# Optimization experiments

Hardware: AMD Instinct MI355X
Metric: run time of the kernel (lower is better)

## Reference

```python
import jax, jax.numpy as jnp
import numpy as np

C = 128          # hidden_channels
H = 8            # num_heads
D = C // H       # head dim = 16
OUT = 64         # out_channels
L = 2            # num_layers
NN = (30000, 60000, 6000)                 # poi, road, region node counts
NE = (200000, 300000, 200000, 100000)     # edges per edge type
ETS = ((0, 1), (1, 1), (1, 2), (2, 0))    # (src_type, dst_type) per edge type


def setup_inputs():
    key = jax.random.key(0)
    ks = iter(jax.random.split(key, 40))
    s = 1.0 / np.sqrt(C)
    sd = 1.0 / np.sqrt(D)
    inp = {}
    inp['x_poi'] = jax.random.normal(next(ks), (NN[0], C), jnp.float32)
    inp['x_road'] = jax.random.normal(next(ks), (NN[1], C), jnp.float32)
    inp['x_region'] = jax.random.normal(next(ks), (NN[2], C), jnp.float32)
    for et, (si, di) in enumerate(ETS):
        inp[f'e{et}_src'] = jax.random.randint(next(ks), (NE[et],), 0, NN[si], jnp.int32)
        inp[f'e{et}_dst'] = jax.random.randint(next(ks), (NE[et],), 0, NN[di], jnp.int32)
    # per-node-type input projection
    inp['lin_w'] = jax.random.normal(next(ks), (3, C, C), jnp.float32) * s
    inp['lin_b'] = jax.random.normal(next(ks), (3, C), jnp.float32) * 0.01
    # per-layer, per-node-type K/Q/V and output projections
    for nm in ('kw', 'qw', 'vw', 'aw'):
        inp[nm] = jax.random.normal(next(ks), (L, 3, C, C), jnp.float32) * s
    for nm in ('kb', 'qb', 'vb', 'ab'):
        inp[nm] = jax.random.normal(next(ks), (L, 3, C), jnp.float32) * 0.01
    # per-layer, per-edge-type relation matrices and priors
    inp['a_rel'] = jax.random.normal(next(ks), (L, 4, H, D, D), jnp.float32) * sd
    inp['m_rel'] = jax.random.normal(next(ks), (L, 4, H, D, D), jnp.float32) * sd
    inp['p_rel'] = jnp.ones((L, 4, H), jnp.float32)
    inp['skip'] = jnp.ones((L, 3), jnp.float32)
    inp['out_w'] = jax.random.normal(next(ks), (C, OUT), jnp.float32) * s
    inp['out_b'] = jnp.zeros((OUT,), jnp.float32)
    return inp


def _seg_softmax(alpha, dst, n):
    amax = jax.lax.stop_gradient(jax.ops.segment_max(alpha, dst, num_segments=n))
    ex = jnp.exp(alpha - amax[dst])
    den = jax.ops.segment_sum(ex, dst, num_segments=n)
    return ex / (den[dst] + 1e-16)


def _hgt_forward(xs, edges, lin_w, lin_b, kw, kb, qw, qb, vw, vb, aw, ab,
                 a_rel, m_rel, p_rel, skip, out_w, out_b):
    # per-node-type input linear + relu
    xs = [jax.nn.relu(xs[i] @ lin_w[i] + lin_b[i]) for i in range(3)]
    scale = 1.0 / np.sqrt(D)
    for l in range(L):
        k = [(xs[i] @ kw[l, i] + kb[l, i]).reshape(-1, H, D) for i in range(3)]
        q = [(xs[i] @ qw[l, i] + qb[l, i]).reshape(-1, H, D) for i in range(3)]
        v = [(xs[i] @ vw[l, i] + vb[l, i]).reshape(-1, H, D) for i in range(3)]
        agg = [jnp.zeros((NN[i], H, D), xs[i].dtype) for i in range(3)]
        for et, (si, di) in enumerate(ETS):
            src, dst = edges[et]
            n = NN[di]
            ke = jnp.einsum('ehd,hdf->ehf', k[si][src], a_rel[l, et])   # [E,H,D]
            alpha = jnp.einsum('ehd,ehd->eh', q[di][dst], ke) * p_rel[l, et] * scale
            alpha = _seg_softmax(alpha, dst, n)                          # [E,H]
            m = jnp.einsum('ehd,hdf->ehf', v[si][src], m_rel[l, et])    # [E,H,D]
            agg[di] = agg[di] + jax.ops.segment_sum(m * alpha[..., None], dst, num_segments=n)
        new_xs = []
        for i in range(3):
            o = jax.nn.gelu(agg[i].reshape(-1, C)) @ aw[l, i] + ab[l, i]
            beta = jax.nn.sigmoid(skip[l, i])
            o = beta * o + (1.0 - beta) * xs[i]
            new_xs.append(jax.nn.relu(o))  # HGT applies activation after each conv
        xs = new_xs
    return (xs[0] @ out_w + out_b, xs[1] @ out_w + out_b, xs[2] @ out_w + out_b)


def reference(x_poi, x_road, x_region,
              e0_src, e0_dst, e1_src, e1_dst, e2_src, e2_dst, e3_src, e3_dst,
              lin_w, lin_b, kw, kb, qw, qb, vw, vb, aw, ab,
              a_rel, m_rel, p_rel, skip, out_w, out_b):
    edges = ((e0_src, e0_dst), (e1_src, e1_dst), (e2_src, e2_dst), (e3_src, e3_dst))
    return _hgt_forward([x_poi, x_road, x_region], edges,
                        lin_w, lin_b, kw, kb, qw, qb, vw, vb, aw, ab,
                        a_rel, m_rel, p_rel, skip, out_w, out_b)
```

## Files before the change

kernel.cpp:

```cpp
#include <hip/hip_runtime.h>
#include <cstddef>
#include <cstdint>


typedef __attribute__((ext_vector_type(8))) short short8;
typedef __attribute__((ext_vector_type(4))) float floatx4;

__device__ __forceinline__ float gelu_fast(float x) {
    float u = 1.5957691216057308f * x * (1.0f + 0.044715f * x * x);
    return x / (1.0f + __expf(-u));
}

__device__ __forceinline__ unsigned short f2bf(float f) {
    unsigned u = __float_as_uint(f);
    u += 0x7fffu + ((u >> 16) & 1);
    return (unsigned short)(u >> 16);
}

__device__ __forceinline__ float bf2f(unsigned short h) {
    return __uint_as_float((unsigned)h << 16);
}

__device__ __forceinline__ void up8(uint4 u, float* f) {
    f[0] = __uint_as_float(u.x << 16); f[1] = __uint_as_float(u.x & 0xffff0000u);
    f[2] = __uint_as_float(u.y << 16); f[3] = __uint_as_float(u.y & 0xffff0000u);
    f[4] = __uint_as_float(u.z << 16); f[5] = __uint_as_float(u.z & 0xffff0000u);
    f[6] = __uint_as_float(u.w << 16); f[7] = __uint_as_float(u.w & 0xffff0000u);
}

__device__ __forceinline__ uint4 pk8(const float* f) {
    uint4 u;
    u.x = (unsigned)f2bf(f[0]) | ((unsigned)f2bf(f[1]) << 16);
    u.y = (unsigned)f2bf(f[2]) | ((unsigned)f2bf(f[3]) << 16);
    u.z = (unsigned)f2bf(f[4]) | ((unsigned)f2bf(f[5]) << 16);
    u.w = (unsigned)f2bf(f[6]) | ((unsigned)f2bf(f[7]) << 16);
    return u;
}

__global__ __launch_bounds__(256) void gemm_proj_all(
    const unsigned short* __restrict__ xs_bf,
    const unsigned short* __restrict__ Wl,
    const float* __restrict__ bl,
    unsigned short* __restrict__ proj)
{
    const int    NN_[3]  = {30000, 60000, 6000};
    const int    OFFr[3] = {0, 30000, 90000};
    const int    WOFF[3] = {0, 49152, 131072};
    const int    BOFF[3] = {0, 384, 1024};
    const size_t POFF[3] = {0, 11520000u, 49920000u};
    const int    LDO[3]  = {384, 640, 384};

    int by = blockIdx.x, t, lb;
    if (by < 2345)      { t = 1; lb = by; }
    else if (by < 3050) { t = 0; lb = by - 2345; }
    else                { t = 2; lb = by - 3050; }
    int XG = (t == 1) ? 5 : 3;
    int byy = lb / XG, bx = lb - byy * XG;

    const unsigned short* Abf = xs_bf + (size_t)OFFr[t] * 128;
    const unsigned short* Wt  = Wl + WOFF[t];
    const float* bias = bl + BOFF[t];
    unsigned short* outbf = proj + POFF[t];
    const int ldo = LDO[t], Nrows = NN_[t];

    const int wave = threadIdx.x >> 6, lane = threadIdx.x & 63;
    const int quad = lane >> 4, l16 = lane & 15;
    const int rowStart = (byy * 4 + wave) * 32;
    if (rowStart >= Nrows) return;
    short8 Afr[2][4];
    #pragma unroll
    for (int rt = 0; rt < 2; ++rt) {
        int m = rowStart + rt * 16 + l16;
        const unsigned short* ap = Abf + (size_t)((m < Nrows) ? m : 0) * 128 + quad * 8;
        #pragma unroll
        for (int kc = 0; kc < 4; ++kc)
            Afr[rt][kc] = *(const short8*)(ap + kc * 32);
    }
    int ct0 = bx * 2, ct1 = ct0 + 2;
    for (int ct = ct0; ct < ct1; ++ct) {
        int colBase = ct * 64;
        const unsigned short* wp = Wt + (size_t)(colBase + l16) * 128 + quad * 8;
        short8 B[4][4];
        #pragma unroll
        for (int c = 0; c < 4; ++c)
            #pragma unroll
            for (int kc = 0; kc < 4; ++kc)
                B[c][kc] = *(const short8*)(wp + (size_t)c * 2048 + kc * 32);
        floatx4 acc[2][4] = {{{0,0,0,0},{0,0,0,0},{0,0,0,0},{0,0,0,0}},
                             {{0,0,0,0},{0,0,0,0},{0,0,0,0},{0,0,0,0}}};
        #pragma unroll
        for (int kc = 0; kc < 4; ++kc)
            #pragma unroll
            for (int c = 0; c < 4; ++c) {
                acc[0][c] = __builtin_amdgcn_mfma_f32_16x16x32_bf16(B[c][kc], Afr[0][kc], acc[0][c], 0, 0, 0);
                acc[1][c] = __builtin_amdgcn_mfma_f32_16x16x32_bf16(B[c][kc], Afr[1][kc], acc[1][c], 0, 0, 0);
            }
        #pragma unroll
        for (int rt = 0; rt < 2; ++rt) {
            int node = rowStart + rt * 16 + l16;
            if (node >= Nrows) continue;
            #pragma unroll
            for (int c = 0; c < 4; ++c) {
                int col0 = colBase + c * 16 + quad * 4;
                float4 bv = *(const float4*)(bias + col0);
                uint2 u;
                u.x = (unsigned)f2bf(acc[rt][c][0] + bv.x) |
                      ((unsigned)f2bf(acc[rt][c][1] + bv.y) << 16);
                u.y = (unsigned)f2bf(acc[rt][c][2] + bv.z) |
                      ((unsigned)f2bf(acc[rt][c][3] + bv.w) << 16);
                *(uint2*)(outbf + (size_t)node * ldo + col0) = u;
            }
        }
    }
}

template<bool AF32, bool GIN, bool SKIP>
__global__ __launch_bounds__(256) void gemm_node(
    const void* __restrict__ a0v, const void* __restrict__ a1v, const void* __restrict__ a2v,
    const unsigned short* __restrict__ WtB, const float* __restrict__ biasB,
    const unsigned short* __restrict__ xoldB, const float* __restrict__ skipB,
    unsigned short* __restrict__ outB)
{
    const int TN[3]   = {30000, 60000, 6000};
    const int TOFF[3] = {0, 30000, 90000};
    int by = blockIdx.x;
    int t  = (by < 469) ? 0 : (by < 1407) ? 1 : 2;
    int lb = by - ((t == 0) ? 0 : (t == 1) ? 469 : 1407);
    int Nrows = TN[t];
    const void* av = (t == 0) ? a0v : (t == 1) ? a1v : a2v;
    const unsigned short* Wt = WtB + (size_t)t * 16384;
    const float* bias = biasB + t * 128;
    const unsigned short* xold = xoldB + (size_t)TOFF[t] * 128;
    unsigned short* out = outB + (size_t)TOFF[t] * 128;
    const int wave = threadIdx.x >> 6, lane = threadIdx.x & 63;
    const int quad = lane >> 4, l16 = lane & 15;
    const int rowStart = (lb * 4 + wave) * 16;
    if (rowStart >= Nrows) return;
    int m = rowStart + l16;
    size_t base = (size_t)((m < Nrows) ? m : 0) * 128 + quad * 8;
    short8 Afr[4];
    #pragma unroll
    for (int kc = 0; kc < 4; ++kc) {
        if (AF32) {
            const float* ap = (const float*)av + base;
            float4 f0 = *(const float4*)(ap + kc * 32);
            float4 f1 = *(const float4*)(ap + kc * 32 + 4);
            float af[8] = {f0.x, f0.y, f0.z, f0.w, f1.x, f1.y, f1.z, f1.w};
            short8 a;
            #pragma unroll
            for (int i = 0; i < 8; ++i) a[i] = (short)f2bf(af[i]);
            Afr[kc] = a;
        } else if (GIN) {
            const unsigned short* ap = (const unsigned short*)av + base;
            short8 a8 = *(const short8*)(ap + kc * 32);
            short8 a;
            #pragma unroll
            for (int i = 0; i < 8; ++i)
                a[i] = (short)f2bf(gelu_fast(bf2f((unsigned short)a8[i])));
            Afr[kc] = a;
        } else {
            const unsigned short* ap = (const unsigned short*)av + base;
            Afr[kc] = *(const short8*)(ap + kc * 32);
        }
    }
    float beta = 0.f, omb = 0.f;
    if (SKIP) { beta = 1.0f / (1.0f + __expf(-skipB[t])); omb = 1.0f - beta; }
    int node = rowStart + l16;
    bool ok = node < Nrows;
    #pragma unroll
    for (int ct = 0; ct < 2; ++ct) {
        int colBase = ct * 64;
        const unsigned short* wp = Wt + (size_t)(colBase + l16) * 128 + quad * 8;
        #pragma unroll
        for (int c = 0; c < 4; ++c) {
            floatx4 acc = {0, 0, 0, 0};
            #pragma unroll
            for (int kc = 0; kc < 4; ++kc) {
                short8 B = *(const short8*)(wp + (size_t)c * 2048 + kc * 32);
                acc = __builtin_amdgcn_mfma_f32_16x16x32_bf16(B, Afr[kc], acc, 0, 0, 0);
            }
            if (ok) {
                int col0 = colBase + c * 16 + quad * 4;
                float4 bv = *(const float4*)(bias + col0);
                float o0 = acc[0] + bv.x, o1 = acc[1] + bv.y;
                float o2 = acc[2] + bv.z, o3 = acc[3] + bv.w;
                if (SKIP) {
                    uint2 xo = *(const uint2*)(xold + (size_t)node * 128 + col0);
                    o0 = beta * o0 + omb * __uint_as_float(xo.x << 16);
                    o1 = beta * o1 + omb * __uint_as_float(xo.x & 0xffff0000u);
                    o2 = beta * o2 + omb * __uint_as_float(xo.y << 16);
                    o3 = beta * o3 + omb * __uint_as_float(xo.y & 0xffff0000u);
                }
                o0 = fmaxf(o0, 0.f); o1 = fmaxf(o1, 0.f);
                o2 = fmaxf(o2, 0.f); o3 = fmaxf(o3, 0.f);
                uint2 u;
                u.x = (unsigned)f2bf(o0) | ((unsigned)f2bf(o1) << 16);
                u.y = (unsigned)f2bf(o2) | ((unsigned)f2bf(o3) << 16);
                *(uint2*)(out + (size_t)node * 128 + col0) = u;
            }
        }
    }
}

__global__ __launch_bounds__(256) void gemm_out(
    const unsigned short* __restrict__ Abf,
    const unsigned short* __restrict__ Wt,
    const float* __restrict__ bias,
    float* __restrict__ out, int Nrows)
{
    const int wave = threadIdx.x >> 6, lane = threadIdx.x & 63;
    const int quad = lane >> 4, l16 = lane & 15;
    const int rowBase = (blockIdx.x * 4 + wave) * 16;
    if (rowBase >= Nrows) return;
    const unsigned short* wp = Wt + (size_t)l16 * 128 + quad * 8;
    int m = rowBase + l16;
    const unsigned short* ap = Abf + (size_t)((m < Nrows) ? m : 0) * 128 + quad * 8;
    short8 Afr[4];
    #pragma unroll
    for (int kc = 0; kc < 4; ++kc) Afr[kc] = *(const short8*)(ap + kc * 32);
    int node = rowBase + l16;
    bool ok = node < Nrows;
    #pragma unroll
    for (int c = 0; c < 4; ++c) {
        floatx4 acc = {0, 0, 0, 0};
        #pragma unroll
        for (int kc = 0; kc < 4; ++kc) {
            short8 B = *(const short8*)(wp + (size_t)c * 2048 + kc * 32);
            acc = __builtin_amdgcn_mfma_f32_16x16x32_bf16(B, Afr[kc], acc, 0, 0, 0);
        }
        if (ok) {
            int col0 = c * 16 + quad * 4;
            float4 bv = *(const float4*)(bias + col0);
            float4 o;
            o.x = acc[0] + bv.x; o.y = acc[1] + bv.y;
            o.z = acc[2] + bv.z; o.w = acc[3] + bv.w;
            *(float4*)(out + (size_t)node * 64 + col0) = o;
        }
    }
}

__global__ __launch_bounds__(128) void prep_qpack(
    const float* __restrict__ qw, const float* __restrict__ qb,
    unsigned short* __restrict__ Wpack, float* __restrict__ bpack)
{
    const int pre[3] = {0, 49152, 131072};
    const int preB[3] = {0, 384, 1024};
    int n = threadIdx.x, k = blockIdx.x, t = blockIdx.y, l = blockIdx.z;
    unsigned short* Wp = Wpack + (size_t)l * 180224 + pre[t];
    Wp[(size_t)n * 128 + k] = f2bf(qw[(size_t)(l * 3 + t) * 16384 + (size_t)k * 128 + n]);
    if (k == 0) bpack[l * 1408 + preB[t] + n] = qb[(l * 3 + t) * 128 + n];
}

__global__ __launch_bounds__(128) void fold_rel_pack(
    const float* __restrict__ kw, const float* __restrict__ kb,
    const float* __restrict__ vw, const float* __restrict__ vb,
    const float* __restrict__ a_rel, const float* __restrict__ m_rel,
    unsigned short* __restrict__ Wpack, float* __restrict__ bpack)
{
    const int SIv[4] = {0, 1, 1, 2};
    const int SLOT[4] = {0, 0, 1, 0};
    const int pre[3] = {0, 49152, 131072};
    const int preB[3] = {0, 384, 1024};
    int hf = threadIdx.x, h = hf >> 4, f = hf & 15;
    int c = blockIdx.x, et = blockIdx.y, l = blockIdx.z;
    int si = SIv[et];
    const float* kwp  = kw + (size_t)(l * 3 + si) * 16384;
    const float* vwp  = vw + (size_t)(l * 3 + si) * 16384;
    const float* kbp  = kb + (size_t)(l * 3 + si) * 128;
    const float* vbp  = vb + (size_t)(l * 3 + si) * 128;
    const float* arel = a_rel + (size_t)(l * 4 + et) * 2048;
    const float* mrel = m_rel + (size_t)(l * 4 + et) * 2048;
    float sk = 0.f, sv = 0.f;
    #pragma unroll
    for (int d = 0; d < 16; ++d) {
        float ar = arel[(h * 16 + d) * 16 + f];
        float mr = mrel[(h * 16 + d) * 16 + f];
        sk = fmaf(kwp[c * 128 + h * 16 + d], ar, sk);
        sv = fmaf(vwp[c * 128 + h * 16 + d], mr, sv);
    }
    int rowoff = 128 + 256 * SLOT[et];
    unsigned short* Wp = Wpack + (size_t)l * 180224 + pre[si];
    Wp[(size_t)(rowoff + hf) * 128 + c]       = f2bf(sk);
    Wp[(size_t)(rowoff + 128 + hf) * 128 + c] = f2bf(sv);
    if (c == 0) {
        float bk = 0.f, bvv = 0.f;
        #pragma unroll
        for (int d = 0; d < 16; ++d) {
            bk  = fmaf(kbp[h * 16 + d], arel[(h * 16 + d) * 16 + f], bk);
            bvv = fmaf(vbp[h * 16 + d], mrel[(h * 16 + d) * 16 + f], bvv);
        }
        float* bp = bpack + l * 1408 + preB[si];
        bp[rowoff + hf]       = bk;
        bp[rowoff + 128 + hf] = bvv;
    }
}

__global__ __launch_bounds__(128) void prep_w9(
    const float* __restrict__ lin_w, const float* __restrict__ aw,
    unsigned short* __restrict__ lwt, unsigned short* __restrict__ awt)
{
    int n = threadIdx.x, k = blockIdx.x, mi = blockIdx.y;
    const float* w; unsigned short* wt; int m;
    if (mi < 3) { w = lin_w; wt = lwt; m = mi; }
    else        { w = aw;    wt = awt; m = mi - 3; }
    wt[(size_t)m * 16384 + (size_t)n * 128 + k] =
        f2bf(w[(size_t)m * 16384 + (size_t)k * 128 + n]);
}

__global__ __launch_bounds__(64) void prep_owt(
    const float* __restrict__ ow, unsigned short* __restrict__ owt)
{
    int n = threadIdx.x, k = blockIdx.x;
    owt[(size_t)n * 128 + k] = f2bf(ow[(size_t)k * 64 + n]);
}

__global__ __launch_bounds__(256) void hist_all(
    const int* __restrict__ d0, const int* __restrict__ d1,
    const int* __restrict__ d2, const int* __restrict__ d3,
    int* __restrict__ deg4)
{
    const int Ev[4] = {200000, 300000, 200000, 100000};
    int et = blockIdx.y;
    int e = blockIdx.x * 256 + threadIdx.x;
    if (e >= Ev[et]) return;
    const int* d = et == 0 ? d0 : et == 1 ? d1 : et == 2 ? d2 : d3;
    atomicAdd(&deg4[et * 60000 + d[e]], 1);
}

__global__ __launch_bounds__(256) void scan_tile_all(
    const int* __restrict__ deg4,
    int* __restrict__ r0, int* __restrict__ r1, int* __restrict__ r2, int* __restrict__ r3,
    int* __restrict__ tsum4)
{
    const int Ndv[4] = {60000, 60000, 6000, 30000};
    __shared__ int ls[256];
    int et = blockIdx.y;
    int n = Ndv[et];
    const int* deg = deg4 + et * 60000;
    int* rowptr = et == 0 ? r0 : et == 1 ? r1 : et == 2 ? r2 : r3;
    int b = blockIdx.x, tid = threadIdx.x;
    int base = b * 1024 + tid * 4;
    int v0 = 0, v1 = 0, v2 = 0, v3 = 0;
    if (base + 3 < n) {
        int4 t = *(const int4*)(deg + base);
        v0 = t.x; v1 = t.y; v2 = t.z; v3 = t.w;
    } else {
        if (base + 0 < n) v0 = deg[base + 0];
        if (base + 1 < n) v1 = deg[base + 1];
        if (base + 2 < n) v2 = deg[base + 2];
        if (base + 3 < n) v3 = deg[base + 3];
    }
    int s = v0 + v1 + v2 + v3;
    ls[tid] = s;
    __syncthreads();
    #pragma unroll
    for (int off = 1; off < 256; off <<= 1) {
        int t = (tid >= off) ? ls[tid - off] : 0;
        __syncthreads();
        ls[tid] += t;
        __syncthreads();
    }
    int run = ls[tid] - s;
    int o0 = run; run += v0;
    int o1 = run; run += v1;
    int o2 = run; run += v2;
    int o3 = run;
    if (base + 3 < n) {
        *(int4*)(rowptr + base) = make_int4(o0, o1, o2, o3);
    } else {
        if (base + 0 < n) rowptr[base + 0] = o0;
        if (base + 1 < n) rowptr[base + 1] = o1;
        if (base + 2 < n) rowptr[base + 2] = o2;
    }
    if (tid == 255) tsum4[et * 64 + b] = ls[255];
}

__global__ __launch_bounds__(64) void scan_tsum_all(
    int* __restrict__ tsum4,
    int* __restrict__ r0, int* __restrict__ r1, int* __restrict__ r2, int* __restrict__ r3)
{
    const int Ndv[4] = {60000, 60000, 6000, 30000};
    int et = blockIdx.x;
    int n = Ndv[et];
    int nt = (n + 1023) >> 10;
    int* tileSum = tsum4 + et * 64;
    int* rowptr = et == 0 ? r0 : et == 1 ? r1 : et == 2 ? r2 : r3;
    int tid = threadIdx.x;
    int v = (tid < nt) ? tileSum[tid] : 0;
    int orig = v;
    #pragma unroll
    for (int off = 1; off < 64; off <<= 1) {
        int t = __shfl_up(v, off);
        if (tid >= off) v += t;
    }
    if (tid < nt) tileSum[tid] = v - orig;
    if (tid == nt - 1) rowptr[n] = v;
}

__global__ __launch_bounds__(256) void scan_add_all(
    int* __restrict__ r0, int* __restrict__ r1, int* __restrict__ r2, int* __restrict__ r3,
    const int* __restrict__ tsum4)
{
    const int Ndv[4] = {60000, 60000, 6000, 30000};
    int et = blockIdx.y;
    int n = Ndv[et];
    int* rowptr = et == 0 ? r0 : et == 1 ? r1 : et == 2 ? r2 : r3;
    int i = blockIdx.x * 256 + threadIdx.x;
    if (i < n) rowptr[i] += tsum4[et * 64 + (i >> 10)];
}

__global__ __launch_bounds__(256) void fill_all(
    const int* __restrict__ s0, const int* __restrict__ d0,
    const int* __restrict__ s1, const int* __restrict__ d1,
    const int* __restrict__ s2, const int* __restrict__ d2,
    const int* __restrict__ s3, const int* __restrict__ d3,
    const int* __restrict__ r0, const int* __restrict__ r1,
    const int* __restrict__ r2, const int* __restrict__ r3,
    int* __restrict__ deg4,
    int* __restrict__ c0, int* __restrict__ c1, int* __restrict__ c2, int* __restrict__ c3)
{
    const int Ev[4] = {200000, 300000, 200000, 100000};
    int et = blockIdx.y;
    int e = blockIdx.x * 256 + threadIdx.x;
    if (e >= Ev[et]) return;
    const int* src = et == 0 ? s0 : et == 1 ? s1 : et == 2 ? s2 : s3;
    const int* dst = et == 0 ? d0 : et == 1 ? d1 : et == 2 ? d2 : d3;
    const int* rowptr = et == 0 ? r0 : et == 1 ? r1 : et == 2 ? r2 : r3;
    int* csr = et == 0 ? c0 : et == 1 ? c1 : et == 2 ? c2 : c3;
    int d = dst[e];
    int pos = atomicAdd(&deg4[et * 60000 + d], 1);
    csr[rowptr[d] + pos] = src[e];
}

__device__ __forceinline__ void attn_run(
    const int* __restrict__ csr, int beg, int end,
    const unsigned short* __restrict__ kbase, int ld,
    const float* qf, float ph, float& m, float& l, float* o)
{
    if (beg >= end) return;
    int s = csr[beg];
    const uint4* kp = (const uint4*)(kbase + (size_t)s * ld);
    uint4 ku0 = kp[0], ku1 = kp[1];
    uint4 vu0 = kp[16], vu1 = kp[17];
    for (int j = beg; j < end; ++j) {
        uint4 nk0 = ku0, nk1 = ku1, nv0 = vu0, nv1 = vu1;
        if (j + 1 < end) {
            int sn = csr[j + 1];
            const uint4* np = (const uint4*)(kbase + (size_t)sn * ld);
            nk0 = np[0]; nk1 = np[1]; nv0 = np[16]; nv1 = np[17];
        }
        float kf[16], vf[16];
        up8(ku0, kf); up8(ku1, kf + 8);
        up8(vu0, vf); up8(vu1, vf + 8);
        float a = 0.f;
        #pragma unroll
        for (int i = 0; i < 16; ++i) a = fmaf(qf[i], kf[i], a);
        a *= ph;
        float d = a - m;
        if (d > 8.f) {
            float sc = __expf(-d);
            l *= sc;
            #pragma unroll
            for (int i = 0; i < 16; ++i) o[i] *= sc;
            m = a; d = 0.f;
        }
        float w = __expf(d);
        l += w;
        #pragma unroll
        for (int i = 0; i < 16; ++i) o[i] = fmaf(w, vf[i], o[i]);
        ku0 = nk0; ku1 = nk1; vu0 = nv0; vu1 = nv1;
    }
}

__global__ __launch_bounds__(256) void agg_all(
    const int* __restrict__ rp0, const int* __restrict__ cs0,
    const int* __restrict__ rp1, const int* __restrict__ cs1,
    const int* __restrict__ rp2, const int* __restrict__ cs2,
    const int* __restrict__ rp3, const int* __restrict__ cs3,
    const unsigned short* __restrict__ P0, const unsigned short* __restrict__ P1,
    const unsigned short* __restrict__ P2,
    const float* __restrict__ prl,
    unsigned short* __restrict__ num)
{
    int gb = blockIdx.x, tid = threadIdx.x;
    float qf[16], o[16], r[16];
    if (gb < 1875) {
        int t = gb * 256 + tid;
        int node = t >> 3, h = t & 7;
        const uint4* qp = (const uint4*)(P1 + (size_t)node * 640 + h * 16);
        up8(qp[0], qf); up8(qp[1], qf + 8);
        float m0 = -INFINITY, l0 = 0.f;
        #pragma unroll
        for (int i = 0; i < 16; ++i) o[i] = 0.f;
        attn_run(cs0, rp0[node], rp0[node + 1], P0 + 128 + h * 16, 384,
                 qf, prl[h] * 0.25f, m0, l0, o);
        float i0 = 1.f / (l0 + 1e-16f);
        #pragma unroll
        for (int i = 0; i < 16; ++i) { r[i] = i0 * o[i]; o[i] = 0.f; }
        float m1 = -INFINITY, l1 = 0.f;
        attn_run(cs1, rp1[node], rp1[node + 1], P1 + 128 + h * 16, 640,
                 qf, prl[8 + h] * 0.25f, m1, l1, o);
        float i1 = 1.f / (l1 + 1e-16f);
        #pragma unroll
        for (int i = 0; i < 16; ++i) r[i] += i1 * o[i];
        uint4* np = (uint4*)(num + (size_t)(30000 + node) * 128 + h * 16);
        np[0] = pk8(r); np[1] = pk8(r + 8);
    } else if (gb < 2625) {
        int t = (gb - 1875) * 256 + tid;
        int node = t >> 5, h = t & 7, sub = (t >> 3) & 3;
        int beg0 = rp2[node], end0 = rp2[node + 1];
        int n = end0 - beg0;
        int beg = beg0 + ((n * sub) >> 2);
        int end = beg0 + ((n * (sub + 1)) >> 2);
        const uint4* qp = (const uint4*)(P2 + (size_t)node * 384 + h * 16);
        up8(qp[0], qf); up8(qp[1], qf + 8);
        float m = -INFINITY, l = 0.f;
        #pragma unroll
        for (int i = 0; i < 16; ++i) o[i] = 0.f;
        attn_run(cs2, beg, end, P1 + 384 + h * 16, 640,
                 qf, prl[16 + h] * 0.25f, m, l, o);
        #pragma unroll
        for (int st = 8; st <= 16; st <<= 1) {
            float mp = __shfl_xor(m, st);
            float lp = __shfl_xor(l, st);
            float mn = fmaxf(m, mp);
            float sc  = (l  > 0.f) ? __expf(m  - mn) : 0.f;
            float scp = (lp > 0.f) ? __expf(mp - mn) : 0.f;
            l = l * sc + lp * scp;
            #pragma unroll
            for (int i = 0; i < 16; ++i) {
                float op = __shfl_xor(o[i], st);
                o[i] = o[i] * sc + op * scp;
            }
            m = mn;
        }
        if (sub) return;
        float inv = 1.f / (l + 1e-16f);
        #pragma unroll
        for (int i = 0; i < 16; ++i) r[i] = inv * o[i];
        uint4* np = (uint4*)(num + (size_t)(90000 + node) * 128 + h * 16);
        np[0] = pk8(r); np[1] = pk8(r + 8);
    } else {
        int t = (gb - 2625) * 256 + tid;
        if (t >= 240000) return;
        int node = t >> 3, h = t & 7;
        const uint4* qp = (const uint4*)(P0 + (size_t)node * 384 + h * 16);
        up8(qp[0], qf); up8(qp[1], qf + 8);
        float m = -INFINITY, l = 0.f;
        #pragma unroll
        for (int i = 0; i < 16; ++i) o[i] = 0.f;
        attn_run(cs3, rp3[node], rp3[node + 1], P2 + 128 + h * 16, 384,
                 qf, prl[24 + h] * 0.25f, m, l, o);
        float inv = 1.f / (l + 1e-16f);
        #pragma unroll
        for (int i = 0; i < 16; ++i) r[i] = inv * o[i];
        uint4* np = (uint4*)(num + (size_t)node * 128 + h * 16);
        np[0] = pk8(r); np[1] = pk8(r + 8);
    }
}

extern "C" void kernel_launch(void* const* d_in, const int* in_sizes, int n_in,
                              void* d_out, int out_size, void* d_ws, size_t ws_size,
                              hipStream_t stream)
{
    (void)in_sizes; (void)n_in; (void)out_size; (void)ws_size;

    const float* xin[3] = {(const float*)d_in[0], (const float*)d_in[1], (const float*)d_in[2]};
    const int* esrc[4] = {(const int*)d_in[3], (const int*)d_in[5], (const int*)d_in[7], (const int*)d_in[9]};
    const int* edst[4] = {(const int*)d_in[4], (const int*)d_in[6], (const int*)d_in[8], (const int*)d_in[10]};
    const float* lin_w = (const float*)d_in[11];
    const float* lin_b = (const float*)d_in[12];
    const float* kw = (const float*)d_in[13];
    const float* qw = (const float*)d_in[14];
    const float* vw = (const float*)d_in[15];
    const float* aw = (const float*)d_in[16];
    const float* kb = (const float*)d_in[17];
    const float* qb = (const float*)d_in[18];
    const float* vb = (const float*)d_in[19];
    const float* ab = (const float*)d_in[20];
    const float* a_rel = (const float*)d_in[21];
    const float* m_rel = (const float*)d_in[22];
    const float* p_rel = (const float*)d_in[23];
    const float* skip  = (const float*)d_in[24];
    const float* out_w = (const float*)d_in[25];
    const float* out_b = (const float*)d_in[26];

    float* ws = (float*)d_ws;
    unsigned short* num   = (unsigned short*)ws;
    unsigned short* xs_bf = (unsigned short*)(ws + 6144000);
    unsigned short* proj  = (unsigned short*)(ws + 12288000);
    unsigned short* Wpack = (unsigned short*)(ws + 38400000);
    unsigned short* lwt   = (unsigned short*)(ws + 38580224);
    unsigned short* awt   = (unsigned short*)(ws + 38604800);
    unsigned short* owt   = (unsigned short*)(ws + 38653952);
    float*          bpack = ws + 38658048;
    int*            deg4  = (int*)(ws + 38660864);
    int*            tsum4 = (int*)(ws + 38900864);
    int* rp[4];
    rp[0] = (int*)(ws + 38901120);
    rp[1] = (int*)(ws + 38961128);
    rp[2] = (int*)(ws + 39021136);
    rp[3] = (int*)(ws + 39027144);
    int* cs[4];
    cs[0] = (int*)(ws + 39057152);
    cs[1] = (int*)(ws + 39257152);
    cs[2] = (int*)(ws + 39557152);
    cs[3] = (int*)(ws + 39757152);

    unsigned short* P[3];
    P[0] = proj;
    P[1] = proj + (size_t)30000 * 384;
    P[2] = proj + (size_t)30000 * 384 + (size_t)60000 * 640;

    dim3 blk(256);

    hipMemsetAsync(deg4, 0, 960000, stream);
    hist_all<<<dim3(1172, 4), blk, 0, stream>>>(edst[0], edst[1], edst[2], edst[3], deg4);
    scan_tile_all<<<dim3(59, 4), blk, 0, stream>>>(deg4, rp[0], rp[1], rp[2], rp[3], tsum4);
    scan_tsum_all<<<dim3(4), dim3(64), 0, stream>>>(tsum4, rp[0], rp[1], rp[2], rp[3]);
    scan_add_all<<<dim3(235, 4), blk, 0, stream>>>(rp[0], rp[1], rp[2], rp[3], tsum4);
    hipMemsetAsync(deg4, 0, 960000, stream);
    fill_all<<<dim3(1172, 4), blk, 0, stream>>>(
        esrc[0], edst[0], esrc[1], edst[1], esrc[2], edst[2], esrc[3], edst[3],
        rp[0], rp[1], rp[2], rp[3], deg4, cs[0], cs[1], cs[2], cs[3]);

    prep_qpack<<<dim3(128, 3, 2), dim3(128), 0, stream>>>(qw, qb, Wpack, bpack);
    fold_rel_pack<<<dim3(128, 4, 2), dim3(128), 0, stream>>>(
        kw, kb, vw, vb, a_rel, m_rel, Wpack, bpack);
    prep_w9<<<dim3(128, 9), dim3(128), 0, stream>>>(lin_w, aw, lwt, awt);
    prep_owt<<<dim3(128), dim3(64), 0, stream>>>(out_w, owt);

    gemm_node<true, false, false><<<dim3(1501), blk, 0, stream>>>(
        xin[0], xin[1], xin[2], lwt, lin_b, nullptr, nullptr, xs_bf);

    for (int l = 0; l < 2; ++l) {
        gemm_proj_all<<<dim3(3191), blk, 0, stream>>>(
            xs_bf, Wpack + (size_t)l * 180224, bpack + l * 1408, proj);

        agg_all<<<dim3(3563), blk, 0, stream>>>(
            rp[0], cs[0], rp[1], cs[1], rp[2], cs[2], rp[3], cs[3],
            P[0], P[1], P[2], p_rel + (size_t)l * 32, num);

        gemm_node<false, true, true><<<dim3(1501), blk, 0, stream>>>(
            num, num + (size_t)30000 * 128, num + (size_t)90000 * 128,
            awt + (size_t)l * 3 * 16384, ab + (size_t)l * 3 * 128,
            xs_bf, skip + l * 3, xs_bf);
    }

    gemm_out<<<dim3(1500), blk, 0, stream>>>(
        xs_bf, owt, out_b, (float*)d_out, 96000);
}
```

Before: 640.9 us.

## Make node GEMMs persistent over row panels with register-resident weights and A prefetch

Restructures the projection, node-update and output GEMM kernels so each block keeps its weight tile in registers and loops over several 64-row panels, prefetching the next panel's activations while running MFMAs on the current one. Grid sizes shrink to match. The aim is to cut repeated weight loads and to hide activation load latency. In exchange the kernels hold more registers and run fewer blocks, which lowers occupancy and load balance.

```diff
diff --git a/kernel.cpp b/kernel.cpp
--- a/kernel.cpp
+++ b/kernel.cpp
@@ -37,159 +37,212 @@
     return u;
 }
 
-__global__ __launch_bounds__(256) void gemm_proj_all(
+__global__ __launch_bounds__(256, 2) void gemm_proj_all(
     const unsigned short* __restrict__ xs_bf,
     const unsigned short* __restrict__ Wl,
     const float* __restrict__ bl,
     unsigned short* __restrict__ proj)
 {
     const int    NN_[3]  = {30000, 60000, 6000};
+    const int    NPAN[3] = {469, 938, 94};
     const int    OFFr[3] = {0, 30000, 90000};
     const int    WOFF[3] = {0, 49152, 131072};
     const int    BOFF[3] = {0, 384, 1024};
     const size_t POFF[3] = {0, 11520000u, 49920000u};
     const int    LDO[3]  = {384, 640, 384};
 
-    int by = blockIdx.x, t, lb;
-    if (by < 2345)      { t = 1; lb = by; }
-    else if (by < 3050) { t = 0; lb = by - 2345; }
-    else                { t = 2; lb = by - 3050; }
-    int XG = (t == 1) ? 5 : 3;
-    int byy = lb / XG, bx = lb - byy * XG;
+    int b = blockIdx.x, t, cp, rb;
+    if (b < 590)      { t = 1; cp = b / 118; rb = b - cp * 118; }
+    else if (b < 767) { int lb = b - 590; t = 0; cp = lb / 59; rb = lb - cp * 59; }
+    else              { int lb = b - 767; t = 2; cp = lb / 12; rb = lb - cp * 12; }
+    int p0 = rb * 8, p1 = p0 + 8;
+    if (p1 > NPAN[t]) p1 = NPAN[t];
 
     const unsigned short* Abf = xs_bf + (size_t)OFFr[t] * 128;
     const unsigned short* Wt  = Wl + WOFF[t];
-    const float* bias = bl + BOFF[t];
+    const float* bias = bl + BOFF[t] + cp * 128;
     unsigned short* outbf = proj + POFF[t];
     const int ldo = LDO[t], Nrows = NN_[t];
 
     const int wave = threadIdx.x >> 6, lane = threadIdx.x & 63;
     const int quad = lane >> 4, l16 = lane & 15;
-    const int rowStart = (byy * 4 + wave) * 32;
-    if (rowStart >= Nrows) return;
-    short8 Afr[2][4];
+
+    short8 B[2][4][4];
+    {
+        const unsigned short* wb = Wt + (size_t)(cp * 128 + l16) * 128 + quad * 8;
+        #pragma unroll
+        for (int T = 0; T < 2; ++T)
+            #pragma unroll
+            for (int c = 0; c < 4; ++c)
+                #pragma unroll
+                for (int kc = 0; kc < 4; ++kc)
+                    B[T][c][kc] = *(const short8*)(wb + (size_t)(T * 64 + c * 16) * 128 + kc * 32);
+    }
+    float4 bv[2][4];
     #pragma unroll
-    for (int rt = 0; rt < 2; ++rt) {
-        int m = rowStart + rt * 16 + l16;
-        const unsigned short* ap = Abf + (size_t)((m < Nrows) ? m : 0) * 128 + quad * 8;
+    for (int T = 0; T < 2; ++T)
+        #pragma unroll
+        for (int c = 0; c < 4; ++c)
+            bv[T][c] = *(const float4*)(bias + T * 64 + c * 16 + quad * 4);
+
+    short8 Acur[4];
+    {
+        int m = p0 * 64 + wave * 16 + l16; if (m >= Nrows) m = Nrows - 1;
+        const unsigned short* ap = Abf + (size_t)m * 128 + quad * 8;
+        #pragma unroll
+        for (int kc = 0; kc < 4; ++kc) Acur[kc] = *(const short8*)(ap + kc * 32);
+    }
+    for (int p = p0; p < p1; ++p) {
+        short8 Anx[4];
+        {
+            int m = (p + 1) * 64 + wave * 16 + l16; if (m >= Nrows) m = Nrows - 1;
+            const unsigned short* ap = Abf + (size_t)m * 128 + quad * 8;
+            #pragma unroll
+            for (int kc = 0; kc < 4; ++kc) Anx[kc] = *(const short8*)(ap + kc * 32);
+        }
+        floatx4 acc[2][4];
+        #pragma unroll
+        for (int T = 0; T < 2; ++T)
+            #pragma unroll
+            for (int c = 0; c < 4; ++c) acc[T][c] = (floatx4){0.f, 0.f, 0.f, 0.f};
         #pragma unroll
         for (int kc = 0; kc < 4; ++kc)
-            Afr[rt][kc] = *(const short8*)(ap + kc * 32);
-    }
-    int ct0 = bx * 2, ct1 = ct0 + 2;
-    for (int ct = ct0; ct < ct1; ++ct) {
-        int colBase = ct * 64;
-        const unsigned short* wp = Wt + (size_t)(colBase + l16) * 128 + quad * 8;
-        short8 B[4][4];
-        #pragma unroll
-        for (int c = 0; c < 4; ++c)
-            #pragma unroll
-            for (int kc = 0; kc < 4; ++kc)
-                B[c][kc] = *(const short8*)(wp + (size_t)c * 2048 + kc * 32);
-        floatx4 acc[2][4] = {{{0,0,0,0},{0,0,0,0},{0,0,0,0},{0,0,0,0}},
-                             {{0,0,0,0},{0,0,0,0},{0,0,0,0},{0,0,0,0}}};
-        #pragma unroll
-        for (int kc = 0; kc < 4; ++kc)
-            #pragma unroll
-            for (int c = 0; c < 4; ++c) {
-                acc[0][c] = __builtin_amdgcn_mfma_f32_16x16x32_bf16(B[c][kc], Afr[0][kc], acc[0][c], 0, 0, 0);
-                acc[1][c] = __builtin_amdgcn_mfma_f32_16x16x32_bf16(B[c][kc], Afr[1][kc], acc[1][c], 0, 0, 0);
-            }
-        #pragma unroll
-        for (int rt = 0; rt < 2; ++rt) {
-            int node = rowStart + rt * 16 + l16;
-            if (node >= Nrows) continue;
-            #pragma unroll
-            for (int c = 0; c < 4; ++c) {
-                int col0 = colBase + c * 16 + quad * 4;
-                float4 bv = *(const float4*)(bias + col0);
-                uint2 u;
-                u.x = (unsigned)f2bf(acc[rt][c][0] + bv.x) |
-                      ((unsigned)f2bf(acc[rt][c][1] + bv.y) << 16);
-                u.y = (unsigned)f2bf(acc[rt][c][2] + bv.z) |
-                      ((unsigned)f2bf(acc[rt][c][3] + bv.w) << 16);
-                *(uint2*)(outbf + (size_t)node * ldo + col0) = u;
-            }
-        }
+            #pragma unroll
+            for (int T = 0; T < 2; ++T)
+                #pragma unroll
+                for (int c = 0; c < 4; ++c)
+                    acc[T][c] = __builtin_amdgcn_mfma_f32_16x16x32_bf16(B[T][c][kc], Acur[kc], acc[T][c], 0, 0, 0);
+        int node = p * 64 + wave * 16 + l16;
+        if (node < Nrows) {
+            unsigned short* op = outbf + (size_t)node * ldo + cp * 128 + quad * 4;
+            #pragma unroll
+            for (int T = 0; T < 2; ++T)
+                #pragma unroll
+                for (int c = 0; c < 4; ++c) {
+                    uint2 u;
+                    u.x = (unsigned)f2bf(acc[T][c][0] + bv[T][c].x) |
+                          ((unsigned)f2bf(acc[T][c][1] + bv[T][c].y) << 16);
+                    u.y = (unsigned)f2bf(acc[T][c][2] + bv[T][c].z) |
+                          ((unsigned)f2bf(acc[T][c][3] + bv[T][c].w) << 16);
+                    *(uint2*)(op + T * 64 + c * 16) = u;
+                }
+        }
+        #pragma unroll
+        for (int kc = 0; kc < 4; ++kc) Acur[kc] = Anx[kc];
     }
 }
 
 template<bool AF32, bool GIN, bool SKIP>
-__global__ __launch_bounds__(256) void gemm_node(
+__global__ __launch_bounds__(256, 2) void gemm_node(
     const void* __restrict__ a0v, const void* __restrict__ a1v, const void* __restrict__ a2v,
     const unsigned short* __restrict__ WtB, const float* __restrict__ biasB,
     const unsigned short* __restrict__ xoldB, const float* __restrict__ skipB,
     unsigned short* __restrict__ outB)
 {
     const int TN[3]   = {30000, 60000, 6000};
+    const int NPAN[3] = {469, 938, 94};
     const int TOFF[3] = {0, 30000, 90000};
-    int by = blockIdx.x;
-    int t  = (by < 469) ? 0 : (by < 1407) ? 1 : 2;
-    int lb = by - ((t == 0) ? 0 : (t == 1) ? 469 : 1407);
+    int b = blockIdx.x, t, rb;
+    if (b < 235)      { t = 0; rb = b; }
+    else if (b < 704) { t = 1; rb = b - 235; }
+    else              { t = 2; rb = b - 704; }
+    int p0 = rb * 2, p1 = p0 + 2;
+    if (p1 > NPAN[t]) p1 = NPAN[t];
     int Nrows = TN[t];
     const void* av = (t == 0) ? a0v : (t == 1) ? a1v : a2v;
-    const unsigned short* Wt = WtB + (size_t)t * 16384;
-    const float* bias = biasB + t * 128;
     const unsigned short* xold = xoldB + (size_t)TOFF[t] * 128;
     unsigned short* out = outB + (size_t)TOFF[t] * 128;
+
     const int wave = threadIdx.x >> 6, lane = threadIdx.x & 63;
     const int quad = lane >> 4, l16 = lane & 15;
-    const int rowStart = (lb * 4 + wave) * 16;
-    if (rowStart >= Nrows) return;
-    int m = rowStart + l16;
-    size_t base = (size_t)((m < Nrows) ? m : 0) * 128 + quad * 8;
-    short8 Afr[4];
-    #pragma unroll
-    for (int kc = 0; kc < 4; ++kc) {
-        if (AF32) {
-            const float* ap = (const float*)av + base;
-            float4 f0 = *(const float4*)(ap + kc * 32);
-            float4 f1 = *(const float4*)(ap + kc * 32 + 4);
-            float af[8] = {f0.x, f0.y, f0.z, f0.w, f1.x, f1.y, f1.z, f1.w};
-            short8 a;
-            #pragma unroll
-            for (int i = 0; i < 8; ++i) a[i] = (short)f2bf(af[i]);
-            Afr[kc] = a;
-        } else if (GIN) {
-            const unsigned short* ap = (const unsigned short*)av + base;
-            short8 a8 = *(const short8*)(ap + kc * 32);
-            short8 a;
-            #pragma unroll
-            for (int i = 0; i < 8; ++i)
-                a[i] = (short)f2bf(gelu_fast(bf2f((unsigned short)a8[i])));
-            Afr[kc] = a;
-        } else {
-            const unsigned short* ap = (const unsigned short*)av + base;
-            Afr[kc] = *(const short8*)(ap + kc * 32);
-        }
+
+    short8 B[8][4];
+    {
+        const unsigned short* wb = WtB + (size_t)t * 16384 + (size_t)l16 * 128 + quad * 8;
+        #pragma unroll
+        for (int c = 0; c < 8; ++c)
+            #pragma unroll
+            for (int kc = 0; kc < 4; ++kc)
+                B[c][kc] = *(const short8*)(wb + (size_t)c * 2048 + kc * 32);
     }
     float beta = 0.f, omb = 0.f;
     if (SKIP) { beta = 1.0f / (1.0f + __expf(-skipB[t])); omb = 1.0f - beta; }
-    int node = rowStart + l16;
-    bool ok = node < Nrows;
-    #pragma unroll
-    for (int ct = 0; ct < 2; ++ct) {
-        int colBase = ct * 64;
-        const unsigned short* wp = Wt + (size_t)(colBase + l16) * 128 + quad * 8;
-        #pragma unroll
-        for (int c = 0; c < 4; ++c) {
-            floatx4 acc = {0, 0, 0, 0};
+
+    short8 Acur[4];
+    {
+        int m = p0 * 64 + wave * 16 + l16; if (m >= Nrows) m = Nrows - 1;
+        size_t base = (size_t)m * 128 + quad * 8;
+        #pragma unroll
+        for (int kc = 0; kc < 4; ++kc) {
+            if (AF32) {
+                const float* ap = (const float*)av + base;
+                float4 f0 = *(const float4*)(ap + kc * 32);
+                float4 f1 = *(const float4*)(ap + kc * 32 + 4);
+                float af[8] = {f0.x, f0.y, f0.z, f0.w, f1.x, f1.y, f1.z, f1.w};
+                short8 a;
+                #pragma unroll
+                for (int i = 0; i < 8; ++i) a[i] = (short)f2bf(af[i]);
+                Acur[kc] = a;
+            } else if (GIN) {
+                const unsigned short* ap = (const unsigned short*)av + base;
+                short8 a8 = *(const short8*)(ap + kc * 32);
+                short8 a;
+                #pragma unroll
+                for (int i = 0; i < 8; ++i)
+                    a[i] = (short)f2bf(gelu_fast(bf2f((unsigned short)a8[i])));
+                Acur[kc] = a;
+            } else {
+                const unsigned short* ap = (const unsigned short*)av + base;
+                Acur[kc] = *(const short8*)(ap + kc * 32);
+            }
+        }
+    }
+    for (int p = p0; p < p1; ++p) {
+        float4 Fnx[4][2];
+        short8 Snx[4];
+        {
+            int m = (p + 1) * 64 + wave * 16 + l16; if (m >= Nrows) m = Nrows - 1;
+            size_t base = (size_t)m * 128 + quad * 8;
             #pragma unroll
             for (int kc = 0; kc < 4; ++kc) {
-                short8 B = *(const short8*)(wp + (size_t)c * 2048 + kc * 32);
-                acc = __builtin_amdgcn_mfma_f32_16x16x32_bf16(B, Afr[kc], acc, 0, 0, 0);
+                if (AF32) {
+                    const float* ap = (const float*)av + base;
+                    Fnx[kc][0] = *(const float4*)(ap + kc * 32);
+                    Fnx[kc][1] = *(const float4*)(ap + kc * 32 + 4);
+                } else {
+                    const unsigned short* ap = (const unsigned short*)av + base;
+                    Snx[kc] = *(const short8*)(ap + kc * 32);
+                }
             }
-            if (ok) {
-                int col0 = colBase + c * 16 + quad * 4;
-                float4 bv = *(const float4*)(bias + col0);
-                float o0 = acc[0] + bv.x, o1 = acc[1] + bv.y;
-                float o2 = acc[2] + bv.z, o3 = acc[3] + bv.w;
+        }
+        int node = p * 64 + wave * 16 + l16;
+        int ncl = (node < Nrows) ? node : (Nrows - 1);
+        uint2 xo[8];
+        if (SKIP) {
+            #pragma unroll
+            for (int c = 0; c < 8; ++c)
+                xo[c] = *(const uint2*)(xold + (size_t)ncl * 128 + c * 16 + quad * 4);
+        }
+        floatx4 acc[8];
+        #pragma unroll
+        for (int c = 0; c < 8; ++c) acc[c] = (floatx4){0.f, 0.f, 0.f, 0.f};
+        #pragma unroll
+        for (int kc = 0; kc < 4; ++kc)
+            #pragma unroll
+            for (int c = 0; c < 8; ++c)
+                acc[c] = __builtin_amdgcn_mfma_f32_16x16x32_bf16(B[c][kc], Acur[kc], acc[c], 0, 0, 0);
+        if (node < Nrows) {
+            #pragma unroll
+            for (int c = 0; c < 8; ++c) {
+                int col0 = c * 16 + quad * 4;
+                float4 bv = *(const float4*)(biasB + t * 128 + col0);
+                float o0 = acc[c][0] + bv.x, o1 = acc[c][1] + bv.y;
+                float o2 = acc[c][2] + bv.z, o3 = acc[c][3] + bv.w;
                 if (SKIP) {
-                    uint2 xo = *(const uint2*)(xold + (size_t)node * 128 + col0);
-                    o0 = beta * o0 + omb * __uint_as_float(xo.x << 16);
-                    o1 = beta * o1 + omb * __uint_as_float(xo.x & 0xffff0000u);
-                    o2 = beta * o2 + omb * __uint_as_float(xo.y << 16);
-                    o3 = beta * o3 + omb * __uint_as_float(xo.y & 0xffff0000u);
+                    o0 = beta * o0 + omb * __uint_as_float(xo[c].x << 16);
+                    o1 = beta * o1 + omb * __uint_as_float(xo[c].x & 0xffff0000u);
+                    o2 = beta * o2 + omb * __uint_as_float(xo[c].y << 16);
+                    o3 = beta * o3 + omb * __uint_as_float(xo[c].y & 0xffff0000u);
                 }
                 o0 = fmaxf(o0, 0.f); o1 = fmaxf(o1, 0.f);
                 o2 = fmaxf(o2, 0.f); o3 = fmaxf(o3, 0.f);
@@ -199,10 +252,29 @@
                 *(uint2*)(out + (size_t)node * 128 + col0) = u;
             }
         }
-    }
-}
-
-__global__ __launch_bounds__(256) void gemm_out(
+        #pragma unroll
+        for (int kc = 0; kc < 4; ++kc) {
+            if (AF32) {
+                float af[8] = {Fnx[kc][0].x, Fnx[kc][0].y, Fnx[kc][0].z, Fnx[kc][0].w,
+                               Fnx[kc][1].x, Fnx[kc][1].y, Fnx[kc][1].z, Fnx[kc][1].w};
+                short8 a;
+                #pragma unroll
+                for (int i = 0; i < 8; ++i) a[i] = (short)f2bf(af[i]);
+                Acur[kc] = a;
+            } else if (GIN) {
+                short8 a;
+                #pragma unroll
+                for (int i = 0; i < 8; ++i)
+                    a[i] = (short)f2bf(gelu_fast(bf2f((unsigned short)Snx[kc][i])));
+                Acur[kc] = a;
+            } else {
+                Acur[kc] = Snx[kc];
+            }
+        }
+    }
+}
+
+__global__ __launch_bounds__(256, 3) void gemm_out(
     const unsigned short* __restrict__ Abf,
     const unsigned short* __restrict__ Wt,
     const float* __restrict__ bias,
@@ -210,32 +282,56 @@
 {
     const int wave = threadIdx.x >> 6, lane = threadIdx.x & 63;
     const int quad = lane >> 4, l16 = lane & 15;
-    const int rowBase = (blockIdx.x * 4 + wave) * 16;
-    if (rowBase >= Nrows) return;
-    const unsigned short* wp = Wt + (size_t)l16 * 128 + quad * 8;
-    int m = rowBase + l16;
-    const unsigned short* ap = Abf + (size_t)((m < Nrows) ? m : 0) * 128 + quad * 8;
-    short8 Afr[4];
+    int p0 = blockIdx.x * 4, p1 = p0 + 4;
+
+    short8 B[4][4];
+    {
+        const unsigned short* wb = Wt + (size_t)l16 * 128 + quad * 8;
+        #pragma unroll
+        for (int c = 0; c < 4; ++c)
+            #pragma unroll
+            for (int kc = 0; kc < 4; ++kc)
+                B[c][kc] = *(const short8*)(wb + (size_t)c * 2048 + kc * 32);
+    }
+    float4 bv[4];
     #pragma unroll
-    for (int kc = 0; kc < 4; ++kc) Afr[kc] = *(const short8*)(ap + kc * 32);
-    int node = rowBase + l16;
-    bool ok = node < Nrows;
-    #pragma unroll
-    for (int c = 0; c < 4; ++c) {
-        floatx4 acc = {0, 0, 0, 0};
-        #pragma unroll
-        for (int kc = 0; kc < 4; ++kc) {
-            short8 B = *(const short8*)(wp + (size_t)c * 2048 + kc * 32);
-            acc = __builtin_amdgcn_mfma_f32_16x16x32_bf16(B, Afr[kc], acc, 0, 0, 0);
-        }
-        if (ok) {
-            int col0 = c * 16 + quad * 4;
-            float4 bv = *(const float4*)(bias + col0);
-            float4 o;
-            o.x = acc[0] + bv.x; o.y = acc[1] + bv.y;
-            o.z = acc[2] + bv.z; o.w = acc[3] + bv.w;
-            *(float4*)(out + (size_t)node * 64 + col0) = o;
-        }
+    for (int c = 0; c < 4; ++c) bv[c] = *(const float4*)(bias + c * 16 + quad * 4);
+
+    short8 Acur[4];
+    {
+        int m = p0 * 64 + wave * 16 + l16; if (m >= Nrows) m = Nrows - 1;
+        const unsigned short* ap = Abf + (size_t)m * 128 + quad * 8;
+        #pragma unroll
+        for (int kc = 0; kc < 4; ++kc) Acur[kc] = *(const short8*)(ap + kc * 32);
+    }
+    for (int p = p0; p < p1; ++p) {
+        short8 Anx[4];
+        {
+            int m = (p + 1) * 64 + wave * 16 + l16; if (m >= Nrows) m = Nrows - 1;
+            const unsigned short* ap = Abf + (size_t)m * 128 + quad * 8;
+            #pragma unroll
+            for (int kc = 0; kc < 4; ++kc) Anx[kc] = *(const short8*)(ap + kc * 32);
+        }
+        floatx4 acc[4];
+        #pragma unroll
+        for (int c = 0; c < 4; ++c) acc[c] = (floatx4){0.f, 0.f, 0.f, 0.f};
+        #pragma unroll
+        for (int kc = 0; kc < 4; ++kc)
+            #pragma unroll
+            for (int c = 0; c < 4; ++c)
+                acc[c] = __builtin_amdgcn_mfma_f32_16x16x32_bf16(B[c][kc], Acur[kc], acc[c], 0, 0, 0);
+        int node = p * 64 + wave * 16 + l16;
+        if (node < Nrows) {
+            #pragma unroll
+            for (int c = 0; c < 4; ++c) {
+                float4 o;
+                o.x = acc[c][0] + bv[c].x; o.y = acc[c][1] + bv[c].y;
+                o.z = acc[c][2] + bv[c].z; o.w = acc[c][3] + bv[c].w;
+                *(float4*)(out + (size_t)node * 64 + c * 16 + quad * 4) = o;
+            }
+        }
+        #pragma unroll
+        for (int kc = 0; kc < 4; ++kc) Acur[kc] = Anx[kc];
     }
 }
 
@@ -630,23 +726,23 @@
     prep_w9<<<dim3(128, 9), dim3(128), 0, stream>>>(lin_w, aw, lwt, awt);
     prep_owt<<<dim3(128), dim3(64), 0, stream>>>(out_w, owt);
 
-    gemm_node<true, false, false><<<dim3(1501), blk, 0, stream>>>(
+    gemm_node<true, false, false><<<dim3(751), blk, 0, stream>>>(
         xin[0], xin[1], xin[2], lwt, lin_b, nullptr, nullptr, xs_bf);
 
     for (int l = 0; l < 2; ++l) {
-        gemm_proj_all<<<dim3(3191), blk, 0, stream>>>(
+        gemm_proj_all<<<dim3(803), blk, 0, stream>>>(
             xs_bf, Wpack + (size_t)l * 180224, bpack + l * 1408, proj);
 
         agg_all<<<dim3(3563), blk, 0, stream>>>(
             rp[0], cs[0], rp[1], cs[1], rp[2], cs[2], rp[3], cs[3],
             P[0], P[1], P[2], p_rel + (size_t)l * 32, num);
 
-        gemm_node<false, true, true><<<dim3(1501), blk, 0, stream>>>(
+        gemm_node<false, true, true><<<dim3(751), blk, 0, stream>>>(
             num, num + (size_t)30000 * 128, num + (size_t)90000 * 128,
             awt + (size_t)l * 3 * 16384, ab + (size_t)l * 3 * 128,
             xs_bf, skip + l * 3, xs_bf);
     }
 
-    gemm_out<<<dim3(1500), blk, 0, stream>>>(
+    gemm_out<<<dim3(375), blk, 0, stream>>>(
         xs_bf, owt, out_b, (float*)d_out, 96000);
 }
```

Measured after the change: 580.6 us. 9.4% less time.
